# Performance work log

Hardware: AMD Instinct MI355X
Metric: run time of the kernel (lower is better)

## Reference

```python
import jax, jax.numpy as jnp
import numpy as np

MAX_AGENTS = 5
AGENT_DIM = 64
NUM_ACTIONS = 10
BATCH = 131072


def setup_inputs() -> dict:
    key = jax.random.key(0)
    ks = jax.random.split(key, 20)
    def lin(k, out_d, in_d):
        kw, kb = jax.random.split(k)
        W = jax.random.normal(kw, (out_d, in_d), jnp.float32) * (1.0 / np.sqrt(in_d))
        b = jax.random.normal(kb, (out_d,), jnp.float32) * 0.02
        return W, b
    x = jax.random.normal(ks[0], (BATCH, MAX_AGENTS * AGENT_DIM), jnp.float32)
    Wk, bk = lin(ks[1], 32, AGENT_DIM)
    Wq, bq = lin(ks[2], 32, AGENT_DIM)
    Wv, bv = lin(ks[3], 64, AGENT_DIM)
    Wr, br = lin(ks[4], 32, 32)
    Wp1, bp1 = lin(ks[5], 64, 64)
    Wp2, bp2 = lin(ks[6], MAX_AGENTS * NUM_ACTIONS, 64)
    Wh1, bh1 = lin(ks[7], 64, 64)
    Wh2, bh2 = lin(ks[8], 1, 64)
    return {"x": x, "Wk": Wk, "bk": bk, "Wq": Wq, "bq": bq, "Wv": Wv, "bv": bv,
            "Wr": Wr, "br": br, "Wp1": Wp1, "bp1": bp1, "Wp2": Wp2, "bp2": bp2,
            "Wh1": Wh1, "bh1": bh1, "Wh2": Wh2, "bh2": bh2}


def reference(x, Wk, bk, Wq, bq, Wv, bv, Wr, br, Wp1, bp1, Wp2, bp2, Wh1, bh1, Wh2, bh2):
    B = x.shape[0]
    agents = x.reshape(B, MAX_AGENTS, AGENT_DIM)  # [B, A, D]
    keys = agents @ Wk.T + bk      # [B, A, 32]
    queries = agents @ Wq.T + bq   # [B, A, 32]
    values = agents @ Wv.T + bv    # [B, A, 64]
    scale = 1.0 / np.sqrt(32.0)
    attn = jnp.einsum('bqd,bkd->bqk', queries, keys) * scale
    rq = queries @ Wr.T + br       # [B, A, 32]
    attn = attn + jnp.einsum('bqd,bkd->bqk', rq, rq) * scale
    attn = jax.nn.softmax(attn, axis=-1)
    context = jnp.einsum('bqk,bkd->bqd', attn, values)  # [B, A, 64]
    agent_mask = (jnp.abs(agents).sum(axis=-1, keepdims=True) > 0.01).astype(x.dtype)  # [B, A, 1]
    pooled = (context * agent_mask).sum(axis=1) / (agent_mask.sum(axis=1) + 1e-8)  # [B, 64]
    h = jax.nn.gelu(pooled @ Wp1.T + bp1, approximate=False)
    action_logits = (h @ Wp2.T + bp2).reshape(B, MAX_AGENTS, NUM_ACTIONS)
    hv = jax.nn.gelu(pooled @ Wh1.T + bh1, approximate=False)
    value = hv @ Wh2.T + bh2  # [B, 1]
    return action_logits, value
```

## Files before the change

kernel.cpp:

```cpp
#include <hip/hip_runtime.h>
#include <stdint.h>


typedef __attribute__((ext_vector_type(8))) short bf16x8;
typedef __attribute__((ext_vector_type(4))) float f32x4;

#define ESTR 168

#define WF1_OFF 0
#define BC_OFF  40960
#define WF2_OFF 41600
#define WF3_OFF 57984

__device__ __forceinline__ float b2f_lo(unsigned int pk) {
  union { unsigned int i; float f; } v; v.i = pk << 16; return v.f;
}
__device__ __forceinline__ float b2f_hi(unsigned int pk) {
  union { unsigned int i; float f; } v; v.i = pk & 0xffff0000u; return v.f;
}
__device__ __forceinline__ float b2f(unsigned short u) {
  union { unsigned int i; float f; } v; v.i = ((unsigned int)u) << 16; return v.f;
}
__device__ __forceinline__ unsigned short f2b(float f) {
  union { float f; unsigned int i; } v; v.f = f;
  unsigned int u = v.i;
  return (unsigned short)((u + 0x7fffu + ((u >> 16) & 1u)) >> 16);
}

__global__ void setup_kernel(const float* __restrict__ Wk,
                             const float* __restrict__ bk,
                             const float* __restrict__ Wq,
                             const float* __restrict__ bq,
                             const float* __restrict__ Wv,
                             const float* __restrict__ bv,
                             const float* __restrict__ Wr,
                             const float* __restrict__ br,
                             const float* __restrict__ Wp1,
                             const float* __restrict__ Wh1,
                             const float* __restrict__ Wp2,
                             char* __restrict__ ws) {
  __shared__ float Wrp[32 * 64];
  const int t = threadIdx.x;
  for (int i = t; i < 32 * 64; i += 256) {
    int rr = i >> 6, d = i & 63;
    float acc = 0.f;
    for (int m = 0; m < 32; ++m) acc += Wr[rr * 32 + m] * Wq[m * 64 + d];
    Wrp[i] = acc;
  }
  __syncthreads();

  unsigned short* wf1 = (unsigned short*)(ws + WF1_OFF);
  float* bc = (float*)(ws + BC_OFF);
  unsigned short* wf2 = (unsigned short*)(ws + WF2_OFF);
  unsigned short* wf3 = (unsigned short*)(ws + WF3_OFF);

  for (int i = t; i < 40 * 64 * 8; i += 256) {
    int j = i & 7, l = (i >> 3) & 63, f = i >> 9;
    int n = f >> 2, h = (f >> 1) & 1, s = f & 1;
    int r = n * 16 + (l & 15);
    int k = s * 32 + ((l >> 4) & 3) * 8 + j;
    float w;
    if (r < 32)      w = Wq[r * 64 + k];
    else if (r < 64) w = Wk[(r - 32) * 64 + k];
    else if (r < 96) w = Wrp[(r - 64) * 64 + k];
    else             w = Wv[(r - 96) * 64 + k];
    unsigned short hi = f2b(w);
    wf1[i] = h ? f2b(w - b2f(hi)) : hi;
  }
  if (t < 160) {
    int r = t;
    float v;
    if (r < 32)      v = bq[r];
    else if (r < 64) v = bk[r - 32];
    else if (r < 96) {
      int rr = r - 64;
      float acc = br[rr];
      for (int m = 0; m < 32; ++m) acc += Wr[rr * 32 + m] * bq[m];
      v = acc;
    } else            v = bv[r - 96];
    bc[r] = v;
  }
  for (int i = t; i < 16 * 64 * 8; i += 256) {
    int j = i & 7, l = (i >> 3) & 63, fs = i >> 9;
    int nt = fs >> 1, s = fs & 1;
    int n = nt * 16 + (l & 15);
    int k = s * 32 + ((l >> 4) & 3) * 8 + j;
    float wv = (n < 64) ? Wp1[n * 64 + k] : Wh1[(n - 64) * 64 + k];
    wf2[i] = f2b(wv);
  }
  for (int i = t; i < 8 * 64 * 8; i += 256) {
    int j = i & 7, l = (i >> 3) & 63, fs = i >> 9;
    int nt = fs >> 1, s = fs & 1;
    int n = nt * 16 + (l & 15);
    int k = s * 32 + ((l >> 4) & 3) * 8 + j;
    float wv = (n < 50) ? Wp2[n * 64 + k] : 0.f;
    wf3[i] = f2b(wv);
  }
}

__global__ __launch_bounds__(512, 2)
void policy_kernel(const float* __restrict__ x,
                   const char* __restrict__ ws,
                   const float* __restrict__ bp1,
                   const float* __restrict__ bp2,
                   const float* __restrict__ bh1,
                   const float* __restrict__ bh2,
                   const float* __restrict__ Wh2,
                   float* __restrict__ out, int B) {
  __shared__ __align__(16) char shpool[74880];
  unsigned short* Els = (unsigned short*)shpool;
  float* maskLs = (float*)(shpool + 53760);
  unsigned short* xfrag = (unsigned short*)(shpool + 54400);
  float* asw  = (float*)(shpool + 54400);
  float* wkLs = (float*)(shpool + 57600);
  float* invLs = (float*)(shpool + 58240);
  unsigned short* pHi = (unsigned short*)(shpool + 58368);
  unsigned short* pLo = (unsigned short*)(shpool + 62464);

  const int t = threadIdx.x;
  const int w = t >> 6, lane = t & 63;
  const int l15 = lane & 15, quad = lane >> 4;

  const uint4* wf1 = (const uint4*)(ws + WF1_OFF);
  const float* bc = (const float*)(ws + BC_OFF);
  const uint4* wf2 = (const uint4*)(ws + WF2_OFF);
  const uint4* wf3 = (const uint4*)(ws + WF3_OFF);

  for (int m = w; m < 10; m += 8) {
    long row = (long)blockIdx.x * 160 + m * 16 + l15;
    const float* xr = x + row * 64 + quad * 8;
    float xv[16];
    *(float4*)(xv + 0)  = *(const float4*)(xr);
    *(float4*)(xv + 4)  = *(const float4*)(xr + 4);
    *(float4*)(xv + 8)  = *(const float4*)(xr + 32);
    *(float4*)(xv + 12) = *(const float4*)(xr + 36);
    float ms = 0.f;
#pragma unroll
    for (int i = 0; i < 16; ++i) ms += fabsf(xv[i]);
    ms += __shfl_xor(ms, 16, 64);
    ms += __shfl_xor(ms, 32, 64);
    if (quad == 0) maskLs[m * 16 + l15] = (ms > 0.01f) ? 1.f : 0.f;
    unsigned int pk[8];
#pragma unroll
    for (int i = 0; i < 8; ++i)
      pk[i] = (unsigned int)f2b(xv[2 * i]) |
              ((unsigned int)f2b(xv[2 * i + 1]) << 16);
    *(uint4*)&xfrag[((m * 2 + 0) * 64 + lane) * 8] =
        make_uint4(pk[0], pk[1], pk[2], pk[3]);
    *(uint4*)&xfrag[((m * 2 + 1) * 64 + lane) * 8] =
        make_uint4(pk[4], pk[5], pk[6], pk[7]);
  }
  __syncthreads();

  {
    union { uint4 u; bf16x8 v; } bh0, bh1, bl0, bl1, a0, a1;
    int ncur = -1;
    float bias = 0.f;
    const int start = (w < 4) ? w * 13 : 52 + (w - 4) * 12;
    const int cnt = (w < 4) ? 13 : 12;
    for (int ti = 0; ti < cnt; ++ti) {
      int tt = start + ti;
      int n = tt / 10, m = tt - n * 10;
      if (n != ncur) {
        ncur = n;
        bh0.u = wf1[(n * 4 + 0) * 64 + lane];
        bh1.u = wf1[(n * 4 + 1) * 64 + lane];
        bl0.u = wf1[(n * 4 + 2) * 64 + lane];
        bl1.u = wf1[(n * 4 + 3) * 64 + lane];
        bias = bc[n * 16 + l15];
      }
      a0.u = *(const uint4*)&xfrag[((m * 2 + 0) * 64 + lane) * 8];
      a1.u = *(const uint4*)&xfrag[((m * 2 + 1) * 64 + lane) * 8];
      f32x4 acc = {0.f, 0.f, 0.f, 0.f};
      acc = __builtin_amdgcn_mfma_f32_16x16x32_bf16(a0.v, bh0.v, acc, 0, 0, 0);
      acc = __builtin_amdgcn_mfma_f32_16x16x32_bf16(a1.v, bh1.v, acc, 0, 0, 0);
      acc = __builtin_amdgcn_mfma_f32_16x16x32_bf16(a0.v, bl0.v, acc, 0, 0, 0);
      acc = __builtin_amdgcn_mfma_f32_16x16x32_bf16(a1.v, bl1.v, acc, 0, 0, 0);
      int r0 = m * 16 + quad * 4;
      int col = n * 16 + l15;
#pragma unroll
      for (int r = 0; r < 4; ++r)
        Els[(r0 + r) * ESTR + col] = f2b(acc[r] + bias);
    }
  }
  __syncthreads();

  for (int ti = w; ti < 11; ti += 8) {
    const unsigned short* ra = &Els[(ti * 15 + l15) * ESTR];
    union { uint4 u; bf16x8 v; } a0, a1, b0;
    a0.u = *(const uint4*)&ra[quad * 8];
    b0.u = *(const uint4*)&ra[32 + quad * 8];
    a1.u = *(const uint4*)&ra[64 + quad * 8];
    f32x4 acc = {0.f, 0.f, 0.f, 0.f};
    acc = __builtin_amdgcn_mfma_f32_16x16x32_bf16(a0.v, b0.v, acc, 0, 0, 0);
    acc = __builtin_amdgcn_mfma_f32_16x16x32_bf16(a1.v, a1.v, acc, 0, 0, 0);
#pragma unroll
    for (int r = 0; r < 4; ++r) {
      int arq = ti * 15 + quad * 4 + r;
      int ark = ti * 15 + l15;
      int bq = arq / 5, qq = arq - 5 * bq;
      int bk2 = ark / 5, kk = ark - 5 * bk2;
      if (bq == bk2 && bq < 32)
        asw[bq * 25 + qq * 5 + kk] = acc[r] * 0.17677669529663689f;
    }
  }
  __syncthreads();

  if (t < 160) {
    const int b = t / 5, k = t - 5 * b;
    const float* ab = &asw[b * 25];
    float wk = 0.f;
#pragma unroll
    for (int q = 0; q < 5; ++q) {
      float s0 = ab[q * 5 + 0], s1 = ab[q * 5 + 1], s2 = ab[q * 5 + 2],
            s3 = ab[q * 5 + 3], s4 = ab[q * 5 + 4];
      float mx = fmaxf(fmaxf(fmaxf(s0, s1), fmaxf(s2, s3)), s4);
      float ps = __expf(s0 - mx) + __expf(s1 - mx) + __expf(s2 - mx) +
                 __expf(s3 - mx) + __expf(s4 - mx);
      float ek = __expf(ab[q * 5 + k] - mx);
      wk += maskLs[b * 5 + q] * __fdividef(ek, ps);
    }
    wkLs[t] = wk;
  }
  if (t < 32) {
    float msum = maskLs[t * 5] + maskLs[t * 5 + 1] + maskLs[t * 5 + 2] +
                 maskLs[t * 5 + 3] + maskLs[t * 5 + 4];
    invLs[t] = 1.0f / (msum + 1e-8f);
  }
  __syncthreads();

  for (int i = t; i < 32 * 64; i += 512) {
    int b = i >> 6, d = i & 63;
    const float* wk = &wkLs[b * 5];
    float acc = 0.f;
#pragma unroll
    for (int k = 0; k < 5; ++k)
      acc = __builtin_fmaf(wk[k], b2f(Els[(5 * b + k) * ESTR + 96 + d]), acc);
    float pv = acc * invLs[b];
    unsigned short hi = f2b(pv);
    unsigned short lo = f2b(pv - b2f(hi));
    int fi = (((b >> 4) * 2 + (d >> 5)) * 64 + ((d >> 3) & 3) * 16 + (b & 15)) * 8
             + (d & 7);
    pHi[fi] = hi; pLo[fi] = lo;
  }
  __syncthreads();

  {
    unsigned short* HHi = (unsigned short*)shpool;
    unsigned short* HLo = (unsigned short*)(shpool + 4096);
    float* Hv = (float*)(shpool + 8192);
    const int mt = w >> 2;
    union { uint4 u; bf16x8 v; } aH0, aH1, aL0, aL1;
    aH0.u = *(const uint4*)&pHi[((mt * 2 + 0) * 64 + lane) * 8];
    aH1.u = *(const uint4*)&pHi[((mt * 2 + 1) * 64 + lane) * 8];
    aL0.u = *(const uint4*)&pLo[((mt * 2 + 0) * 64 + lane) * 8];
    aL1.u = *(const uint4*)&pLo[((mt * 2 + 1) * 64 + lane) * 8];
#pragma unroll
    for (int tI = 0; tI < 2; ++tI) {
      int nt = (w & 3) * 2 + tI;
      union { uint4 u; bf16x8 v; } b0, b1;
      b0.u = wf2[(nt * 2 + 0) * 64 + lane];
      b1.u = wf2[(nt * 2 + 1) * 64 + lane];
      f32x4 acc = {0.f, 0.f, 0.f, 0.f};
      acc = __builtin_amdgcn_mfma_f32_16x16x32_bf16(aL0.v, b0.v, acc, 0, 0, 0);
      acc = __builtin_amdgcn_mfma_f32_16x16x32_bf16(aL1.v, b1.v, acc, 0, 0, 0);
      acc = __builtin_amdgcn_mfma_f32_16x16x32_bf16(aH0.v, b0.v, acc, 0, 0, 0);
      acc = __builtin_amdgcn_mfma_f32_16x16x32_bf16(aH1.v, b1.v, acc, 0, 0, 0);
      int col = nt * 16 + l15;
      float bias = (col < 64) ? bp1[col] : bh1[col - 64];
#pragma unroll
      for (int r = 0; r < 4; ++r) {
        int row = mt * 16 + quad * 4 + r;
        float v = acc[r] + bias;
        float g = 0.5f * v * (1.0f + erff(v * 0.70710678118654752f));
        if (col < 64) {
          unsigned short hi = f2b(g);
          unsigned short lo = f2b(g - b2f(hi));
          int fi = ((mt * 2 + (col >> 5)) * 64 + ((col >> 3) & 3) * 16 + (row & 15)) * 8
                   + (col & 7);
          HHi[fi] = hi; HLo[fi] = lo;
        } else {
          Hv[row * 65 + (col - 64)] = g;
        }
      }
    }
  }
  __syncthreads();

  {
    const unsigned short* HHi = (const unsigned short*)shpool;
    const unsigned short* HLo = (const unsigned short*)(shpool + 4096);
    const float* Hv = (const float*)(shpool + 8192);
    const int mt = w >> 2, nt = w & 3;
    union { uint4 u; bf16x8 v; } aH0, aH1, aL0, aL1, b0, b1;
    aH0.u = *(const uint4*)&HHi[((mt * 2 + 0) * 64 + lane) * 8];
    aH1.u = *(const uint4*)&HHi[((mt * 2 + 1) * 64 + lane) * 8];
    aL0.u = *(const uint4*)&HLo[((mt * 2 + 0) * 64 + lane) * 8];
    aL1.u = *(const uint4*)&HLo[((mt * 2 + 1) * 64 + lane) * 8];
    b0.u = wf3[(nt * 2 + 0) * 64 + lane];
    b1.u = wf3[(nt * 2 + 1) * 64 + lane];
    f32x4 acc = {0.f, 0.f, 0.f, 0.f};
    acc = __builtin_amdgcn_mfma_f32_16x16x32_bf16(aL0.v, b0.v, acc, 0, 0, 0);
    acc = __builtin_amdgcn_mfma_f32_16x16x32_bf16(aL1.v, b1.v, acc, 0, 0, 0);
    acc = __builtin_amdgcn_mfma_f32_16x16x32_bf16(aH0.v, b0.v, acc, 0, 0, 0);
    acc = __builtin_amdgcn_mfma_f32_16x16x32_bf16(aH1.v, b1.v, acc, 0, 0, 0);
    int col = nt * 16 + l15;
    if (col < 50) {
      float bias = bp2[col];
#pragma unroll
      for (int r = 0; r < 4; ++r) {
        int row = mt * 16 + quad * 4 + r;
        long gb = (long)blockIdx.x * 32 + row;
        out[gb * 50 + col] = acc[r] + bias;
      }
    }
    if (t < 32) {
      float s = bh2[0];
#pragma unroll
      for (int j = 0; j < 64; ++j)
        s = __builtin_fmaf(Hv[t * 65 + j], Wh2[j], s);
      out[(long)B * 50 + (long)blockIdx.x * 32 + t] = s;
    }
  }
}

extern "C" void kernel_launch(void* const* d_in, const int* in_sizes, int n_in,
                              void* d_out, int out_size, void* d_ws, size_t ws_size,
                              hipStream_t stream) {
  const float* x   = (const float*)d_in[0];
  const float* Wk  = (const float*)d_in[1];
  const float* bk  = (const float*)d_in[2];
  const float* Wq  = (const float*)d_in[3];
  const float* bq  = (const float*)d_in[4];
  const float* Wv  = (const float*)d_in[5];
  const float* bv  = (const float*)d_in[6];
  const float* Wr  = (const float*)d_in[7];
  const float* br  = (const float*)d_in[8];
  const float* Wp1 = (const float*)d_in[9];
  const float* bp1 = (const float*)d_in[10];
  const float* Wp2 = (const float*)d_in[11];
  const float* bp2 = (const float*)d_in[12];
  const float* Wh1 = (const float*)d_in[13];
  const float* bh1 = (const float*)d_in[14];
  const float* Wh2 = (const float*)d_in[15];
  const float* bh2 = (const float*)d_in[16];

  int B = in_sizes[0] / 320;

  setup_kernel<<<1, 256, 0, stream>>>(Wk, bk, Wq, bq, Wv, bv, Wr, br,
                                      Wp1, Wh1, Wp2, (char*)d_ws);
  policy_kernel<<<B / 32, 512, 0, stream>>>(x, (const char*)d_ws,
                                            bp1, bp2, bh1, bh2, Wh2,
                                            (float*)d_out, B);
}
```

Before: 348.0 us.

## Parallelize weight setup, fold biases into MFMA accumulators, fuse value head into output GEMM

Splits the single-block setup kernel into two multi-block kernels so weight packing runs across many workgroups. In the main kernel, MFMA operands are swapped so each lane gets four consecutive columns, allowing biases to be preloaded into the accumulator and results stored as packed 8-byte writes. The value head's 64-wide dot product is folded into the final GEMM as an extra output column of a widened K=128 weight, removing the serial per-thread loop and the fp32 Hv buffer. It adds an extra kernel launch and more zero-padded MFMA work in the last stage.

```diff
diff --git a/kernel.cpp b/kernel.cpp
--- a/kernel.cpp
+++ b/kernel.cpp
@@ -6,11 +6,15 @@
 typedef __attribute__((ext_vector_type(4))) float f32x4;
 
 #define ESTR 168
+#define HSTR 136
 
 #define WF1_OFF 0
 #define BC_OFF  40960
 #define WF2_OFF 41600
 #define WF3_OFF 57984
+#define BMLP_OFF 74368
+#define BCOMB_OFF 74880
+#define WRP_OFF 75136
 
 __device__ __forceinline__ float b2f_lo(unsigned int pk) {
   union { unsigned int i; float f; } v; v.i = pk << 16; return v.f;
@@ -27,34 +31,46 @@
   return (unsigned short)((u + 0x7fffu + ((u >> 16) & 1u)) >> 16);
 }
 
-__global__ void setup_kernel(const float* __restrict__ Wk,
-                             const float* __restrict__ bk,
-                             const float* __restrict__ Wq,
-                             const float* __restrict__ bq,
-                             const float* __restrict__ Wv,
-                             const float* __restrict__ bv,
-                             const float* __restrict__ Wr,
-                             const float* __restrict__ br,
-                             const float* __restrict__ Wp1,
-                             const float* __restrict__ Wh1,
-                             const float* __restrict__ Wp2,
-                             char* __restrict__ ws) {
-  __shared__ float Wrp[32 * 64];
-  const int t = threadIdx.x;
-  for (int i = t; i < 32 * 64; i += 256) {
-    int rr = i >> 6, d = i & 63;
-    float acc = 0.f;
-    for (int m = 0; m < 32; ++m) acc += Wr[rr * 32 + m] * Wq[m * 64 + d];
-    Wrp[i] = acc;
-  }
-  __syncthreads();
-
+__global__ void setup_a(const float* __restrict__ Wr,
+                        const float* __restrict__ Wq,
+                        char* __restrict__ ws) {
+  int id = blockIdx.x * 256 + threadIdx.x;
+  if (id >= 32 * 64) return;
+  int rr = id >> 6, d = id & 63;
+  float acc = 0.f;
+#pragma unroll 8
+  for (int m = 0; m < 32; ++m) acc += Wr[rr * 32 + m] * Wq[m * 64 + d];
+  ((float*)(ws + WRP_OFF))[id] = acc;
+}
+
+__global__ void setup_b(const float* __restrict__ Wk,
+                        const float* __restrict__ bk,
+                        const float* __restrict__ Wq,
+                        const float* __restrict__ bq,
+                        const float* __restrict__ Wv,
+                        const float* __restrict__ bv,
+                        const float* __restrict__ Wr,
+                        const float* __restrict__ br,
+                        const float* __restrict__ Wp1,
+                        const float* __restrict__ bp1,
+                        const float* __restrict__ Wh1,
+                        const float* __restrict__ bh1,
+                        const float* __restrict__ Wp2,
+                        const float* __restrict__ bp2,
+                        const float* __restrict__ Wh2,
+                        const float* __restrict__ bh2,
+                        char* __restrict__ ws) {
+  const float* Wrp = (const float*)(ws + WRP_OFF);
   unsigned short* wf1 = (unsigned short*)(ws + WF1_OFF);
   float* bc = (float*)(ws + BC_OFF);
   unsigned short* wf2 = (unsigned short*)(ws + WF2_OFF);
   unsigned short* wf3 = (unsigned short*)(ws + WF3_OFF);
-
-  for (int i = t; i < 40 * 64 * 8; i += 256) {
+  float* bmlp = (float*)(ws + BMLP_OFF);
+  float* bcomb = (float*)(ws + BCOMB_OFF);
+
+  int gid = blockIdx.x * 256 + threadIdx.x;
+  if (gid < 20480) {
+    int i = gid;
     int j = i & 7, l = (i >> 3) & 63, f = i >> 9;
     int n = f >> 2, h = (f >> 1) & 1, s = f & 1;
     int r = n * 16 + (l & 15);
@@ -66,46 +82,51 @@
     else             w = Wv[(r - 96) * 64 + k];
     unsigned short hi = f2b(w);
     wf1[i] = h ? f2b(w - b2f(hi)) : hi;
-  }
-  if (t < 160) {
-    int r = t;
-    float v;
-    if (r < 32)      v = bq[r];
-    else if (r < 64) v = bk[r - 32];
-    else if (r < 96) {
-      int rr = r - 64;
-      float acc = br[rr];
-      for (int m = 0; m < 32; ++m) acc += Wr[rr * 32 + m] * bq[m];
-      v = acc;
-    } else            v = bv[r - 96];
-    bc[r] = v;
-  }
-  for (int i = t; i < 16 * 64 * 8; i += 256) {
+  } else if (gid < 28672) {
+    int i = gid - 20480;
     int j = i & 7, l = (i >> 3) & 63, fs = i >> 9;
     int nt = fs >> 1, s = fs & 1;
     int n = nt * 16 + (l & 15);
     int k = s * 32 + ((l >> 4) & 3) * 8 + j;
     float wv = (n < 64) ? Wp1[n * 64 + k] : Wh1[(n - 64) * 64 + k];
     wf2[i] = f2b(wv);
-  }
-  for (int i = t; i < 8 * 64 * 8; i += 256) {
-    int j = i & 7, l = (i >> 3) & 63, fs = i >> 9;
-    int nt = fs >> 1, s = fs & 1;
-    int n = nt * 16 + (l & 15);
+  } else if (gid < 36864) {
+    int i = gid - 28672;
+    int j = i & 7, l = (i >> 3) & 63, f = i >> 9;
+    int nt = f >> 2, s = f & 3;
+    int o = nt * 16 + (l & 15);
     int k = s * 32 + ((l >> 4) & 3) * 8 + j;
-    float wv = (n < 50) ? Wp2[n * 64 + k] : 0.f;
+    float wv = 0.f;
+    if (o < 50 && k < 64)        wv = Wp2[o * 64 + k];
+    else if (o == 50 && k >= 64) wv = Wh2[k - 64];
     wf3[i] = f2b(wv);
+  } else {
+    int sid = gid - 36864;
+    if (sid < 160) {
+      int r = sid;
+      float v;
+      if (r < 32)      v = bq[r];
+      else if (r < 64) v = bk[r - 32];
+      else if (r < 96) {
+        int rr = r - 64;
+        float acc = br[rr];
+        for (int m = 0; m < 32; ++m) acc += Wr[rr * 32 + m] * bq[m];
+        v = acc;
+      } else            v = bv[r - 96];
+      bc[r] = v;
+    } else if (sid < 288) {
+      int c = sid - 160;
+      bmlp[c] = (c < 64) ? bp1[c] : bh1[c - 64];
+    } else if (sid < 352) {
+      int o = sid - 288;
+      bcomb[o] = (o < 50) ? bp2[o] : ((o == 50) ? bh2[0] : 0.f);
+    }
   }
 }
 
 __global__ __launch_bounds__(512, 2)
 void policy_kernel(const float* __restrict__ x,
                    const char* __restrict__ ws,
-                   const float* __restrict__ bp1,
-                   const float* __restrict__ bp2,
-                   const float* __restrict__ bh1,
-                   const float* __restrict__ bh2,
-                   const float* __restrict__ Wh2,
                    float* __restrict__ out, int B) {
   __shared__ __align__(16) char shpool[74880];
   unsigned short* Els = (unsigned short*)shpool;
@@ -116,6 +137,8 @@
   float* invLs = (float*)(shpool + 58240);
   unsigned short* pHi = (unsigned short*)(shpool + 58368);
   unsigned short* pLo = (unsigned short*)(shpool + 62464);
+  unsigned short* HHi = (unsigned short*)shpool;
+  unsigned short* HLo = (unsigned short*)(shpool + 8704);
 
   const int t = threadIdx.x;
   const int w = t >> 6, lane = t & 63;
@@ -125,6 +148,8 @@
   const float* bc = (const float*)(ws + BC_OFF);
   const uint4* wf2 = (const uint4*)(ws + WF2_OFF);
   const uint4* wf3 = (const uint4*)(ws + WF3_OFF);
+  const float* bmlp = (const float*)(ws + BMLP_OFF);
+  const float* bcomb = (const float*)(ws + BCOMB_OFF);
 
   for (int m = w; m < 10; m += 8) {
     long row = (long)blockIdx.x * 160 + m * 16 + l15;
@@ -153,9 +178,9 @@
   __syncthreads();
 
   {
-    union { uint4 u; bf16x8 v; } bh0, bh1, bl0, bl1, a0, a1;
+    union { uint4 u; bf16x8 v; } ah0, ah1, al0, al1, b0, b1;
     int ncur = -1;
-    float bias = 0.f;
+    float4 bb = {0.f, 0.f, 0.f, 0.f};
     const int start = (w < 4) ? w * 13 : 52 + (w - 4) * 12;
     const int cnt = (w < 4) ? 13 : 12;
     for (int ti = 0; ti < cnt; ++ti) {
@@ -163,24 +188,25 @@
       int n = tt / 10, m = tt - n * 10;
       if (n != ncur) {
         ncur = n;
-        bh0.u = wf1[(n * 4 + 0) * 64 + lane];
-        bh1.u = wf1[(n * 4 + 1) * 64 + lane];
-        bl0.u = wf1[(n * 4 + 2) * 64 + lane];
-        bl1.u = wf1[(n * 4 + 3) * 64 + lane];
-        bias = bc[n * 16 + l15];
+        ah0.u = wf1[(n * 4 + 0) * 64 + lane];
+        ah1.u = wf1[(n * 4 + 1) * 64 + lane];
+        al0.u = wf1[(n * 4 + 2) * 64 + lane];
+        al1.u = wf1[(n * 4 + 3) * 64 + lane];
+        bb = *(const float4*)&bc[n * 16 + quad * 4];
       }
-      a0.u = *(const uint4*)&xfrag[((m * 2 + 0) * 64 + lane) * 8];
-      a1.u = *(const uint4*)&xfrag[((m * 2 + 1) * 64 + lane) * 8];
-      f32x4 acc = {0.f, 0.f, 0.f, 0.f};
-      acc = __builtin_amdgcn_mfma_f32_16x16x32_bf16(a0.v, bh0.v, acc, 0, 0, 0);
-      acc = __builtin_amdgcn_mfma_f32_16x16x32_bf16(a1.v, bh1.v, acc, 0, 0, 0);
-      acc = __builtin_amdgcn_mfma_f32_16x16x32_bf16(a0.v, bl0.v, acc, 0, 0, 0);
-      acc = __builtin_amdgcn_mfma_f32_16x16x32_bf16(a1.v, bl1.v, acc, 0, 0, 0);
-      int r0 = m * 16 + quad * 4;
-      int col = n * 16 + l15;
-#pragma unroll
-      for (int r = 0; r < 4; ++r)
-        Els[(r0 + r) * ESTR + col] = f2b(acc[r] + bias);
+      b0.u = *(const uint4*)&xfrag[((m * 2 + 0) * 64 + lane) * 8];
+      b1.u = *(const uint4*)&xfrag[((m * 2 + 1) * 64 + lane) * 8];
+      f32x4 acc = {bb.x, bb.y, bb.z, bb.w};
+      acc = __builtin_amdgcn_mfma_f32_16x16x32_bf16(ah0.v, b0.v, acc, 0, 0, 0);
+      acc = __builtin_amdgcn_mfma_f32_16x16x32_bf16(ah1.v, b1.v, acc, 0, 0, 0);
+      acc = __builtin_amdgcn_mfma_f32_16x16x32_bf16(al0.v, b0.v, acc, 0, 0, 0);
+      acc = __builtin_amdgcn_mfma_f32_16x16x32_bf16(al1.v, b1.v, acc, 0, 0, 0);
+      unsigned int u0 = (unsigned int)f2b(acc[0]) |
+                        ((unsigned int)f2b(acc[1]) << 16);
+      unsigned int u1 = (unsigned int)f2b(acc[2]) |
+                        ((unsigned int)f2b(acc[3]) << 16);
+      *(uint2*)&Els[(m * 16 + l15) * ESTR + n * 16 + quad * 4] =
+          make_uint2(u0, u1);
     }
   }
   __syncthreads();
@@ -229,97 +255,89 @@
   }
   __syncthreads();
 
-  for (int i = t; i < 32 * 64; i += 512) {
-    int b = i >> 6, d = i & 63;
+  for (int i = t; i < 32 * 32; i += 512) {
+    int b = i >> 5, d0 = (i & 31) * 2;
     const float* wk = &wkLs[b * 5];
-    float acc = 0.f;
-#pragma unroll
-    for (int k = 0; k < 5; ++k)
-      acc = __builtin_fmaf(wk[k], b2f(Els[(5 * b + k) * ESTR + 96 + d]), acc);
-    float pv = acc * invLs[b];
-    unsigned short hi = f2b(pv);
-    unsigned short lo = f2b(pv - b2f(hi));
-    int fi = (((b >> 4) * 2 + (d >> 5)) * 64 + ((d >> 3) & 3) * 16 + (b & 15)) * 8
-             + (d & 7);
-    pHi[fi] = hi; pLo[fi] = lo;
+    float a0 = 0.f, a1 = 0.f;
+#pragma unroll
+    for (int k = 0; k < 5; ++k) {
+      unsigned int v = *(const unsigned int*)&Els[(5 * b + k) * ESTR + 96 + d0];
+      a0 = __builtin_fmaf(wk[k], b2f_lo(v), a0);
+      a1 = __builtin_fmaf(wk[k], b2f_hi(v), a1);
+    }
+    float inv = invLs[b];
+    float p0 = a0 * inv, p1 = a1 * inv;
+    unsigned short h0 = f2b(p0), h1 = f2b(p1);
+    unsigned short l0 = f2b(p0 - b2f(h0)), l1 = f2b(p1 - b2f(h1));
+    int fi = (((b >> 4) * 2 + (d0 >> 5)) * 64 + ((d0 >> 3) & 3) * 16 + (b & 15))
+                 * 8 + (d0 & 7);
+    *(unsigned int*)&pHi[fi] = (unsigned int)h0 | ((unsigned int)h1 << 16);
+    *(unsigned int*)&pLo[fi] = (unsigned int)l0 | ((unsigned int)l1 << 16);
   }
   __syncthreads();
 
   {
-    unsigned short* HHi = (unsigned short*)shpool;
-    unsigned short* HLo = (unsigned short*)(shpool + 4096);
-    float* Hv = (float*)(shpool + 8192);
     const int mt = w >> 2;
-    union { uint4 u; bf16x8 v; } aH0, aH1, aL0, aL1;
-    aH0.u = *(const uint4*)&pHi[((mt * 2 + 0) * 64 + lane) * 8];
-    aH1.u = *(const uint4*)&pHi[((mt * 2 + 1) * 64 + lane) * 8];
-    aL0.u = *(const uint4*)&pLo[((mt * 2 + 0) * 64 + lane) * 8];
-    aL1.u = *(const uint4*)&pLo[((mt * 2 + 1) * 64 + lane) * 8];
+    union { uint4 u; bf16x8 v; } pH0, pH1, pL0, pL1;
+    pH0.u = *(const uint4*)&pHi[((mt * 2 + 0) * 64 + lane) * 8];
+    pH1.u = *(const uint4*)&pHi[((mt * 2 + 1) * 64 + lane) * 8];
+    pL0.u = *(const uint4*)&pLo[((mt * 2 + 0) * 64 + lane) * 8];
+    pL1.u = *(const uint4*)&pLo[((mt * 2 + 1) * 64 + lane) * 8];
 #pragma unroll
     for (int tI = 0; tI < 2; ++tI) {
-      int nt = (w & 3) * 2 + tI;
-      union { uint4 u; bf16x8 v; } b0, b1;
-      b0.u = wf2[(nt * 2 + 0) * 64 + lane];
-      b1.u = wf2[(nt * 2 + 1) * 64 + lane];
-      f32x4 acc = {0.f, 0.f, 0.f, 0.f};
-      acc = __builtin_amdgcn_mfma_f32_16x16x32_bf16(aL0.v, b0.v, acc, 0, 0, 0);
-      acc = __builtin_amdgcn_mfma_f32_16x16x32_bf16(aL1.v, b1.v, acc, 0, 0, 0);
-      acc = __builtin_amdgcn_mfma_f32_16x16x32_bf16(aH0.v, b0.v, acc, 0, 0, 0);
-      acc = __builtin_amdgcn_mfma_f32_16x16x32_bf16(aH1.v, b1.v, acc, 0, 0, 0);
-      int col = nt * 16 + l15;
-      float bias = (col < 64) ? bp1[col] : bh1[col - 64];
+      int cht = (w & 3) * 2 + tI;
+      union { uint4 u; bf16x8 v; } aw0, aw1;
+      aw0.u = wf2[(cht * 2 + 0) * 64 + lane];
+      aw1.u = wf2[(cht * 2 + 1) * 64 + lane];
+      float4 bb = *(const float4*)&bmlp[cht * 16 + quad * 4];
+      f32x4 acc = {bb.x, bb.y, bb.z, bb.w};
+      acc = __builtin_amdgcn_mfma_f32_16x16x32_bf16(aw0.v, pH0.v, acc, 0, 0, 0);
+      acc = __builtin_amdgcn_mfma_f32_16x16x32_bf16(aw1.v, pH1.v, acc, 0, 0, 0);
+      acc = __builtin_amdgcn_mfma_f32_16x16x32_bf16(aw0.v, pL0.v, acc, 0, 0, 0);
+      acc = __builtin_amdgcn_mfma_f32_16x16x32_bf16(aw1.v, pL1.v, acc, 0, 0, 0);
+      unsigned short hi[4], lo[4];
 #pragma unroll
       for (int r = 0; r < 4; ++r) {
-        int row = mt * 16 + quad * 4 + r;
-        float v = acc[r] + bias;
+        float v = acc[r];
         float g = 0.5f * v * (1.0f + erff(v * 0.70710678118654752f));
-        if (col < 64) {
-          unsigned short hi = f2b(g);
-          unsigned short lo = f2b(g - b2f(hi));
-          int fi = ((mt * 2 + (col >> 5)) * 64 + ((col >> 3) & 3) * 16 + (row & 15)) * 8
-                   + (col & 7);
-          HHi[fi] = hi; HLo[fi] = lo;
-        } else {
-          Hv[row * 65 + (col - 64)] = g;
-        }
+        hi[r] = f2b(g);
+        lo[r] = f2b(g - b2f(hi[r]));
       }
+      int base = (mt * 16 + l15) * HSTR + cht * 16 + quad * 4;
+      *(uint2*)&HHi[base] = make_uint2(
+          (unsigned int)hi[0] | ((unsigned int)hi[1] << 16),
+          (unsigned int)hi[2] | ((unsigned int)hi[3] << 16));
+      *(uint2*)&HLo[base] = make_uint2(
+          (unsigned int)lo[0] | ((unsigned int)lo[1] << 16),
+          (unsigned int)lo[2] | ((unsigned int)lo[3] << 16));
     }
   }
   __syncthreads();
 
   {
-    const unsigned short* HHi = (const unsigned short*)shpool;
-    const unsigned short* HLo = (const unsigned short*)(shpool + 4096);
-    const float* Hv = (const float*)(shpool + 8192);
     const int mt = w >> 2, nt = w & 3;
-    union { uint4 u; bf16x8 v; } aH0, aH1, aL0, aL1, b0, b1;
-    aH0.u = *(const uint4*)&HHi[((mt * 2 + 0) * 64 + lane) * 8];
-    aH1.u = *(const uint4*)&HHi[((mt * 2 + 1) * 64 + lane) * 8];
-    aL0.u = *(const uint4*)&HLo[((mt * 2 + 0) * 64 + lane) * 8];
-    aL1.u = *(const uint4*)&HLo[((mt * 2 + 1) * 64 + lane) * 8];
-    b0.u = wf3[(nt * 2 + 0) * 64 + lane];
-    b1.u = wf3[(nt * 2 + 1) * 64 + lane];
-    f32x4 acc = {0.f, 0.f, 0.f, 0.f};
-    acc = __builtin_amdgcn_mfma_f32_16x16x32_bf16(aL0.v, b0.v, acc, 0, 0, 0);
-    acc = __builtin_amdgcn_mfma_f32_16x16x32_bf16(aL1.v, b1.v, acc, 0, 0, 0);
-    acc = __builtin_amdgcn_mfma_f32_16x16x32_bf16(aH0.v, b0.v, acc, 0, 0, 0);
-    acc = __builtin_amdgcn_mfma_f32_16x16x32_bf16(aH1.v, b1.v, acc, 0, 0, 0);
-    int col = nt * 16 + l15;
-    if (col < 50) {
-      float bias = bp2[col];
-#pragma unroll
-      for (int r = 0; r < 4; ++r) {
-        int row = mt * 16 + quad * 4 + r;
-        long gb = (long)blockIdx.x * 32 + row;
-        out[gb * 50 + col] = acc[r] + bias;
-      }
-    }
-    if (t < 32) {
-      float s = bh2[0];
-#pragma unroll
-      for (int j = 0; j < 64; ++j)
-        s = __builtin_fmaf(Hv[t * 65 + j], Wh2[j], s);
-      out[(long)B * 50 + (long)blockIdx.x * 32 + t] = s;
+    const int row = mt * 16 + l15;
+    union { uint4 u; bf16x8 v; } a[4], bh[4], bl[4];
+#pragma unroll
+    for (int s = 0; s < 4; ++s) {
+      a[s].u = wf3[(nt * 4 + s) * 64 + lane];
+      bh[s].u = *(const uint4*)&HHi[row * HSTR + s * 32 + quad * 8];
+      bl[s].u = *(const uint4*)&HLo[row * HSTR + s * 32 + quad * 8];
+    }
+    float4 bb = *(const float4*)&bcomb[nt * 16 + quad * 4];
+    f32x4 acc = {bb.x, bb.y, bb.z, bb.w};
+#pragma unroll
+    for (int s = 0; s < 4; ++s) {
+      acc = __builtin_amdgcn_mfma_f32_16x16x32_bf16(a[s].v, bh[s].v, acc, 0, 0, 0);
+      acc = __builtin_amdgcn_mfma_f32_16x16x32_bf16(a[s].v, bl[s].v, acc, 0, 0, 0);
+    }
+    long gb = (long)blockIdx.x * 32 + row;
+    int o0 = nt * 16 + quad * 4;
+#pragma unroll
+    for (int r = 0; r < 4; ++r) {
+      int o = o0 + r;
+      if (o < 50)       out[gb * 50 + o] = acc[r];
+      else if (o == 50) out[(long)B * 50 + gb] = acc[r];
     }
   }
 }
@@ -347,9 +365,10 @@
 
   int B = in_sizes[0] / 320;
 
-  setup_kernel<<<1, 256, 0, stream>>>(Wk, bk, Wq, bq, Wv, bv, Wr, br,
-                                      Wp1, Wh1, Wp2, (char*)d_ws);
+  setup_a<<<8, 256, 0, stream>>>(Wr, Wq, (char*)d_ws);
+  setup_b<<<145, 256, 0, stream>>>(Wk, bk, Wq, bq, Wv, bv, Wr, br,
+                                   Wp1, bp1, Wh1, bh1, Wp2, bp2, Wh2, bh2,
+                                   (char*)d_ws);
   policy_kernel<<<B / 32, 512, 0, stream>>>(x, (const char*)d_ws,
-                                            bp1, bp2, bh1, bh2, Wh2,
                                             (float*)d_out, B);
 }
```

After: 313.9 us. 9.8% less time.
